# Kernel tuning notes

Hardware: AMD Instinct MI355X
Metric: run time of the kernel (lower is better)

## Reference

```python
import jax, jax.numpy as jnp
import numpy as np

DIM = 512; HEADS = 8; DHEAD = 64; INNER = HEADS * DHEAD
T = 9; H = 16; W = 16; KS = 5; KT = 7
SEQ = T * H * W + 1          # 2305 tokens incl. BOS
GH = 48; GW = 48             # axial grid: sqrt(T*H*W) = 48
B = 2


def _nearby_mask_np():
    """Faithful numpy port of generate_nearby_mask(causal=True). True = masked."""
    te = (KT - 1) // 2
    frame = H * W
    S = T * frame
    pad = KS // 2
    tmpl = (np.arange(KS * KS) >= (KS * KS) // 2).reshape(KS, KS)
    mb = np.ones((S, T, H + 2 * pad, W + 2 * pad), dtype=bool)
    for t in range(T):
        for h in range(H):
            for w in range(W):
                i = t * frame + h * W + w
                mb[i, t, h:h + KS, w:w + KS] = tmpl
                mb[i, max(0, t - te):t, h:h + KS, w:w + KS] = False
    mb = mb[:, :, pad:-pad, pad:-pad].reshape(S, S)
    mb = np.roll(mb, -1, axis=0)
    out = np.ones((S + 1, S + 1), dtype=bool)  # pad 1 row/col of True at top-left
    out[1:, 1:] = mb
    out[0, 0] = False
    return out


def setup_inputs() -> dict:
    key = jax.random.key(0)
    ks = jax.random.split(key, 16)
    inp = {
        "x": jax.random.normal(ks[0], (B, SEQ, DIM), jnp.float32),
        "nearby_mask": jnp.asarray(_nearby_mask_np()),
    }
    i = 1
    for l in range(3):
        for nm in ("Wq", "Wk", "Wv", "Wo"):
            inp[f"{nm}{l}"] = jax.random.normal(ks[i], (DIM, INNER), jnp.float32) * 0.02
            i += 1
        inp[f"bo{l}"] = jnp.zeros((DIM,), jnp.float32)
    return inp


def _neg(dt):
    return -jnp.finfo(dt).max


def _axial(x, Wq, Wk, Wv, Wo, bo, typ):
    # type 0: attend along rows (width axis); type 1: attend along columns.
    b = x.shape[0]
    scale = DHEAD ** -0.5
    q, k, v = x @ Wq, x @ Wk, x @ Wv

    def split(t):
        bos = t[:, :1].reshape(b, 1, HEADS, DHEAD).transpose(0, 2, 1, 3)[:, :, None]  # b hd 1 1 d
        img = t[:, 1:].reshape(b, GH, GW, HEADS, DHEAD)
        if typ == 0:
            img = img.transpose(0, 3, 1, 2, 4)  # b hd h w d
            nq = GH
        else:
            img = img.transpose(0, 3, 2, 1, 4)  # b hd w h d
            nq = GW
        bos = jnp.broadcast_to(bos, (b, HEADS, nq, 1, DHEAD))
        return jnp.concatenate([bos, img], axis=3)  # b hd nq (1+len) d

    qs, ks, vs = split(q), split(k), split(v)
    dots = jnp.einsum('bhnid,bhnjd->bhnij', qs, ks) * scale
    L = dots.shape[-1]
    causal = jnp.triu(jnp.ones((L, L), dtype=bool), 1)
    dots = jnp.where(causal, _neg(dots.dtype), dots)
    attn = jax.nn.softmax(dots, axis=-1)
    out = jnp.einsum('bhnij,bhnjd->bhnid', attn, vs)
    out_bos = out[:, :, 0, 0].reshape(b, 1, INNER)
    oi = out[:, :, :, 1:, :]
    if typ == 0:
        oi = oi.transpose(0, 2, 3, 1, 4).reshape(b, GH * GW, INNER)  # b (h w) (hd d)
    else:
        oi = oi.transpose(0, 3, 2, 1, 4).reshape(b, GH * GW, INNER)
    return jnp.concatenate([out_bos, oi], axis=1) @ Wo + bo


def _nearby(x, Wq, Wk, Wv, Wo, bo, mask):
    b, n, _ = x.shape
    scale = DHEAD ** -0.5
    q = (x @ Wq).reshape(b, n, HEADS, DHEAD).transpose(0, 2, 1, 3)
    k = (x @ Wk).reshape(b, n, HEADS, DHEAD).transpose(0, 2, 1, 3)
    v = (x @ Wv).reshape(b, n, HEADS, DHEAD).transpose(0, 2, 1, 3)
    dots = jnp.einsum('bhid,bhjd->bhij', q, k) * scale
    dots = jnp.where(mask, _neg(dots.dtype), dots)
    attn = jax.nn.softmax(dots, axis=-1)
    out = jnp.einsum('bhij,bhjd->bhid', attn, v)
    return out.transpose(0, 2, 1, 3).reshape(b, n, INNER) @ Wo + bo


def reference(x, nearby_mask,
              Wq0, Wk0, Wv0, Wo0, bo0,
              Wq1, Wk1, Wv1, Wo1, bo1,
              Wq2, Wk2, Wv2, Wo2, bo2):
    x = x + _axial(x, Wq0, Wk0, Wv0, Wo0, bo0, 0)   # row axial
    x = x + _axial(x, Wq1, Wk1, Wv1, Wo1, bo1, 1)   # column axial
    x = x + _nearby(x, Wq2, Wk2, Wv2, Wo2, bo2, nearby_mask)  # nearby sparse-mask attn
    return x
```

## Files before the change

kernel.cpp:

```cpp
#include <hip/hip_runtime.h>
#include <hip/hip_bf16.h>

#define SEQ 2305
#define NROWS 4610
#define MPAD 4736
#define DIM 512
#define QKVN 1536

typedef __attribute__((ext_vector_type(8))) short v8s;
typedef __attribute__((ext_vector_type(4))) float v4f;

__device__ __forceinline__ float bf2f(unsigned short u) {
    return __uint_as_float(((unsigned)u) << 16);
}

__device__ __forceinline__ void load_lds16(const void* g, void* l) {
    __builtin_amdgcn_global_load_lds(
        (const __attribute__((address_space(1))) void*)g,
        (__attribute__((address_space(3))) void*)l, 16, 0, 0);
}

struct WPack { const float* p[12]; };

__global__ void prep_inputs(WPack wp, __hip_bfloat16* __restrict__ wqkv,
                            __hip_bfloat16* __restrict__ wo,
                            const float4* __restrict__ xin,
                            __hip_bfloat16* __restrict__ xb, int n4,
                            float* __restrict__ colsum) {
    int tx = threadIdx.x, ty = threadIdx.y;
    int m = blockIdx.z;
    if (m == 12) {
        int tidl = ty * 32 + tx;
        int bid = blockIdx.y * 16 + blockIdx.x;
        if (bid == 0) {
            #pragma unroll
            for (int k = 0; k < 4; k++) colsum[k * 256 + tidl] = 0.f;
        }
        for (int i = bid * 256 + tidl; i < n4; i += 65536) {
            float4 v = xin[i];
            int j = i * 4;
            xb[j + 0] = __float2bfloat16(v.x);
            xb[j + 1] = __float2bfloat16(v.y);
            xb[j + 2] = __float2bfloat16(v.z);
            xb[j + 3] = __float2bfloat16(v.w);
        }
        return;
    }
    __shared__ float tile[32][33];
    const float* src = wp.p[m];
    int l = m >> 2, j = m & 3;
    __hip_bfloat16* dst = (j < 3) ? (wqkv + (size_t)l * QKVN * DIM + (size_t)j * DIM * DIM)
                                  : (wo + (size_t)l * DIM * DIM);
    int bx = blockIdx.x * 32, by = blockIdx.y * 32;
    #pragma unroll
    for (int i = 0; i < 4; i++)
        tile[ty + 8 * i][tx] = src[(size_t)(by + ty + 8 * i) * DIM + bx + tx];
    __syncthreads();
    #pragma unroll
    for (int i = 0; i < 4; i++)
        dst[(size_t)(bx + ty + 8 * i) * DIM + by + tx] = __float2bfloat16(tile[tx][ty + 8 * i]);
}

__global__ __launch_bounds__(256) void gemm_lds(
    const __hip_bfloat16* __restrict__ A, const __hip_bfloat16* __restrict__ Bt,
    float* __restrict__ C, const float* __restrict__ bias,
    const __hip_bfloat16* __restrict__ resb, __hip_bfloat16* __restrict__ Cb,
    int M, int N, float* __restrict__ colsum) {
    __shared__ short As[2][64 * 32];
    __shared__ short Bs[2][128 * 32];
    const int K = 512;
    int tid = threadIdx.x;
    int wid = tid >> 6, lane = tid & 63;
    int quad = lane >> 4, l16 = lane & 15;
    int bM = blockIdx.x * 64, bN = blockIdx.y * 128;
    int wM = (wid >> 1) * 32, wN = (wid & 1) * 64;

    const short* Ag = (const short*)A;
    const short* Bg = (const short*)Bt;

    int rowS = tid >> 2, cg = tid & 3;
    const short* gA = Ag + (size_t)(bM + rowS) * K + cg * 8;
    const short* gB0 = Bg + (size_t)(bN + rowS) * K + cg * 8;
    const short* gB1 = Bg + (size_t)(bN + 64 + rowS) * K + cg * 8;

    v4f acc[2][4] = {};
    for (int k0 = 0; k0 < K; k0 += 64) {
        #pragma unroll
        for (int s = 0; s < 2; s++) {
            load_lds16(gA + k0 + s * 32, As[s] + wid * 512);
            load_lds16(gB0 + k0 + s * 32, Bs[s] + wid * 512);
            load_lds16(gB1 + k0 + s * 32, Bs[s] + 2048 + wid * 512);
        }
        __syncthreads();
        #pragma unroll
        for (int s = 0; s < 2; s++) {
            v8s af[2], bf[4];
            #pragma unroll
            for (int i = 0; i < 2; i++)
                af[i] = *(const v8s*)(As[s] + (wM + i * 16 + l16) * 32 + quad * 8);
            #pragma unroll
            for (int j = 0; j < 4; j++)
                bf[j] = *(const v8s*)(Bs[s] + (wN + j * 16 + l16) * 32 + quad * 8);
            #pragma unroll
            for (int i = 0; i < 2; i++)
                #pragma unroll
                for (int j = 0; j < 4; j++)
                    acc[i][j] = __builtin_amdgcn_mfma_f32_16x16x32_bf16(af[i], bf[j], acc[i][j], 0, 0, 0);
        }
        __syncthreads();
    }

    const unsigned short* resu = (const unsigned short*)resb;
    #pragma unroll
    for (int i = 0; i < 2; i++) {
        int row = bM + wM + i * 16 + quad * 4;
        #pragma unroll
        for (int j = 0; j < 4; j++) {
            int col = bN + wN + j * 16 + l16;
            #pragma unroll
            for (int r = 0; r < 4; r++) {
                int rr = row + r;
                if (rr < M) {
                    float v = acc[i][j][r];
                    if (bias) v += bias[col];
                    size_t idx = (size_t)rr * N + col;
                    if (resu) v += bf2f(resu[idx]);
                    if (C) C[idx] = v;
                    if (Cb) Cb[idx] = __float2bfloat16(v);
                }
            }
        }
    }

    if (colsum) {
        #pragma unroll
        for (int j = 0; j < 4; j++) {
            int col = bN + wN + j * 16 + l16;
            if (col >= 1024) {
                float s0 = 0.f, s1 = 0.f;
                #pragma unroll
                for (int i = 0; i < 2; i++) {
                    int row = bM + wM + i * 16 + quad * 4;
                    #pragma unroll
                    for (int r = 0; r < 4; r++) {
                        int rr = row + r;
                        if (rr < M) {
                            float v = acc[i][j][r];
                            if (rr >= SEQ) s1 += v; else s0 += v;
                        }
                    }
                }
                s0 += __shfl_xor(s0, 16); s0 += __shfl_xor(s0, 32);
                s1 += __shfl_xor(s1, 16); s1 += __shfl_xor(s1, 32);
                if (quad == 0) {
                    if (s0 != 0.f) atomicAdd(&colsum[col - 1024], s0);
                    if (s1 != 0.f) atomicAdd(&colsum[512 + col - 1024], s1);
                }
            }
        }
    }
}

__global__ __launch_bounds__(256) void axial_flash(
    const unsigned short* __restrict__ qkvb, __hip_bfloat16* __restrict__ attn_b, int typ) {
    __shared__ short Ks[64 * 64];
    __shared__ short Vs[64 * 64];
    __shared__ short Ps[64 * 72];
    __shared__ float invl[64];

    int tid = threadIdx.x;
    int wid = tid >> 6, lane = tid & 63;
    int quad = lane >> 4, l16 = lane & 15;
    int n = blockIdx.x;
    int b = blockIdx.y >> 3, h = blockIdx.y & 7;
    size_t rowbase = (size_t)b * SEQ;
    int hoff = h * 64;

    #pragma unroll
    for (int it = 0; it < 2; it++) {
        int linear = it * 256 + tid;
        int slot = linear >> 3;
        int cd = linear & 7;
        int cs = cd ^ (slot & 7);
        int sp = (slot == 0) ? 0
               : (slot <= 48 ? (typ == 0 ? 1 + n * 48 + (slot - 1) : 1 + (slot - 1) * 48 + n) : 0);
        const unsigned short* srcK = qkvb + (rowbase + sp) * QKVN + hoff + 512 + cs * 8;
        load_lds16(srcK, Ks + it * 2048 + wid * 512 + lane * 8);
        const unsigned short* srcV = qkvb + (rowbase + sp) * QKVN + hoff + 1024 + cd * 8;
        load_lds16(srcV, Vs + it * 2048 + wid * 512 + lane * 8);
    }

    int qi = wid * 16 + l16;
    int sp_q = (qi >= 1 && qi <= 48)
             ? (typ == 0 ? 1 + n * 48 + (qi - 1) : 1 + (qi - 1) * 48 + n) : 0;
    const unsigned short* qptr = qkvb + (rowbase + sp_q) * QKVN + hoff + quad * 8;
    v8s qa0 = *(const v8s*)qptr;
    v8s qa1 = *(const v8s*)(qptr + 32);

    __syncthreads();

    if (n == 0 && tid < 64) {
        attn_b[rowbase * DIM + hoff + tid] =
            __float2bfloat16(bf2f(qkvb[rowbase * QKVN + hoff + 1024 + tid]));
    }

    v4f st[4];
    #pragma unroll
    for (int kt = 0; kt < 4; kt++) {
        int slot = kt * 16 + l16;
        int s7 = slot & 7;
        v8s blo = *(const v8s*)(Ks + slot * 64 + ((quad ^ s7) * 8));
        v8s bhi = *(const v8s*)(Ks + slot * 64 + (((4 + quad) ^ s7) * 8));
        v4f a = {};
        a = __builtin_amdgcn_mfma_f32_16x16x32_bf16(qa0, blo, a, 0, 0, 0);
        a = __builtin_amdgcn_mfma_f32_16x16x32_bf16(qa1, bhi, a, 0, 0, 0);
        st[kt] = a;
    }

    const float NEG = -3.0e38f;
    float sv[4][4];
    float pm[4] = {NEG, NEG, NEG, NEG};
    #pragma unroll
    for (int kt = 0; kt < 4; kt++) {
        int j = kt * 16 + l16;
        #pragma unroll
        for (int r = 0; r < 4; r++) {
            int i = wid * 16 + quad * 4 + r;
            bool ok = (i >= 1) && (i <= 48) && (j <= i);
            float v = ok ? st[kt][r] * 0.125f : NEG;
            sv[kt][r] = v;
            pm[r] = fmaxf(pm[r], v);
        }
    }
    #pragma unroll
    for (int r = 0; r < 4; r++)
        for (int o = 1; o < 16; o <<= 1) pm[r] = fmaxf(pm[r], __shfl_xor(pm[r], o));

    float ps[4] = {0.f, 0.f, 0.f, 0.f};
    #pragma unroll
    for (int kt = 0; kt < 4; kt++) {
        int j = kt * 16 + l16;
        #pragma unroll
        for (int r = 0; r < 4; r++) {
            float e = __expf(sv[kt][r] - pm[r]);
            ps[r] += e;
            Ps[(wid * 16 + quad * 4 + r) * 72 + j] = (short)__bfloat16_as_ushort(__float2bfloat16(e));
        }
    }
    #pragma unroll
    for (int r = 0; r < 4; r++)
        for (int o = 1; o < 16; o <<= 1) ps[r] += __shfl_xor(ps[r], o);
    if (l16 == 0) {
        #pragma unroll
        for (int r = 0; r < 4; r++)
            invl[wid * 16 + quad * 4 + r] = 1.0f / ps[r];
    }
    __syncthreads();

    #pragma unroll
    for (int qt = 0; qt < 4; qt++) {
        v4f oc = {};
        #pragma unroll
        for (int kc = 0; kc < 2; kc++) {
            v8s pa = *(const v8s*)(Ps + (qt * 16 + l16) * 72 + kc * 32 + quad * 8);
            v8s bfr;
            #pragma unroll
            for (int jj = 0; jj < 8; jj++)
                bfr[jj] = Vs[(kc * 32 + quad * 8 + jj) * 64 + wid * 16 + l16];
            oc = __builtin_amdgcn_mfma_f32_16x16x32_bf16(pa, bfr, oc, 0, 0, 0);
        }
        #pragma unroll
        for (int r = 0; r < 4; r++) {
            int i = qt * 16 + quad * 4 + r;
            if (i >= 1 && i <= 48) {
                int sp = typ == 0 ? 1 + n * 48 + (i - 1) : 1 + (i - 1) * 48 + n;
                attn_b[(rowbase + sp) * DIM + hoff + wid * 16 + l16] =
                    __float2bfloat16(oc[r] * invl[i]);
            }
        }
    }
}

__global__ __launch_bounds__(256) void nearby_flash(
    const unsigned short* __restrict__ qkvb, const float* __restrict__ colsum,
    __hip_bfloat16* __restrict__ attn_b) {
    __shared__ short Vs[128 * 64];
    __shared__ __hip_bfloat16 Ps[16 * 264];
    __shared__ float redm[16 * 4];
    __shared__ float reds[16 * 4];

    int tid = threadIdx.x;
    int wid = tid >> 6, lane = tid & 63;
    int quad = lane >> 4, l16 = lane & 15;

    int idx = blockIdx.x;
    if (idx >= 2304) {
        int b = idx - 2304;
        size_t rb = (size_t)b * SEQ;
        for (int c = tid; c < 512; c += 256) {
            attn_b[(rb + 2304) * DIM + c] =
                __float2bfloat16(colsum[b * 512 + c] * (1.0f / 2305.0f));
            attn_b[rb * DIM + c] =
                __float2bfloat16(bf2f(qkvb[rb * QKVN + 1024 + c]));
        }
        return;
    }

    int bh = idx & 15;
    int tile = idx >> 4;
    int b = bh >> 3, h = bh & 7;
    int t = tile >> 4;
    int sxy = tile & 15;
    int hh0 = (sxy >> 2) * 4, ww0 = (sxy & 3) * 4;
    int nf = (t < 3 ? t : 3) + 1;
    int t0 = t - (nf - 1);
    size_t rowbase = (size_t)b * SEQ;
    int hoff = h * 64;

    auto slot_kp = [&](int slot) -> int {
        int f = slot >> 6, uy = (slot >> 3) & 7, ux = slot & 7;
        int kh = hh0 - 2 + uy, kw = ww0 - 2 + ux;
        int kt = t0 + f;
        bool ok = (kh >= 0) && (kh < 16) && (kw >= 0) && (kw < 16) && (f < nf);
        return ok ? (kt * 256 + kh * 16 + kw + 1) : 0;
    };

    int qp_f = t * 256 + (hh0 + (l16 >> 2)) * 16 + (ww0 + (l16 & 3));
    const unsigned short* qptr = qkvb + (rowbase + qp_f) * QKVN + hoff + quad * 8;
    v8s qa0 = *(const v8s*)qptr;
    v8s qa1 = *(const v8s*)(qptr + 32);

    v8s kb_lo[4], kb_hi[4];
    #pragma unroll
    for (int k = 0; k < 4; k++) {
        int slot = (wid * 4 + k) * 16 + l16;
        int kp = slot_kp(slot);
        const unsigned short* kr = qkvb + (rowbase + kp) * QKVN + hoff + 512;
        kb_lo[k] = *(const v8s*)(kr + quad * 8);
        kb_hi[k] = *(const v8s*)(kr + 32 + quad * 8);
    }

    #pragma unroll
    for (int it = 0; it < 4; it++) {
        int linear = it * 256 + tid;
        int slot = linear >> 3;
        int cd = linear & 7;
        int cs = cd ^ ((slot >> 3) & 7);
        int kp = slot_kp(slot);
        const unsigned short* src = qkvb + (rowbase + kp) * QKVN + hoff + 1024 + cs * 8;
        load_lds16(src, Vs + it * 2048 + wid * 512 + lane * 8);
    }

    v4f st[4];
    #pragma unroll
    for (int k = 0; k < 4; k++) {
        v4f a = {};
        a = __builtin_amdgcn_mfma_f32_16x16x32_bf16(qa0, kb_lo[k], a, 0, 0, 0);
        a = __builtin_amdgcn_mfma_f32_16x16x32_bf16(qa1, kb_hi[k], a, 0, 0, 0);
        st[k] = a;
    }

    const float NEG = -3.0e38f;
    float sv[4][4];
    float pm[4] = {NEG, NEG, NEG, NEG};
    #pragma unroll
    for (int k = 0; k < 4; k++) {
        int slot = (wid * 4 + k) * 16 + l16;
        int f = slot >> 6, uy = (slot >> 3) & 7, ux = slot & 7;
        int kh = hh0 - 2 + uy, kw = ww0 - 2 + ux;
        bool okb = (kh >= 0) && (kh < 16) && (kw >= 0) && (kw < 16) && (f < nf);
        int dyp2 = uy - quad;
        bool oky = okb && (dyp2 >= 0) && (dyp2 <= 4);
        #pragma unroll
        for (int r = 0; r < 4; r++) {
            int dxp2 = ux - r;
            bool ok = oky && (dxp2 >= 0) && (dxp2 <= 4);
            if (f == nf - 1) ok = ok && (dyp2 * 5 + dxp2 < 12);
            float v = ok ? st[k][r] * 0.125f : NEG;
            sv[k][r] = v;
            pm[r] = fmaxf(pm[r], v);
        }
    }
    #pragma unroll
    for (int r = 0; r < 4; r++)
        for (int o = 1; o < 16; o <<= 1) pm[r] = fmaxf(pm[r], __shfl_xor(pm[r], o));
    if (l16 == 0) {
        #pragma unroll
        for (int r = 0; r < 4; r++) redm[(quad * 4 + r) * 4 + wid] = pm[r];
    }
    __syncthreads();

    float rm[4];
    #pragma unroll
    for (int r = 0; r < 4; r++) {
        int row = (quad * 4 + r) * 4;
        rm[r] = fmaxf(fmaxf(redm[row], redm[row + 1]), fmaxf(redm[row + 2], redm[row + 3]));
    }

    float ps[4] = {0.f, 0.f, 0.f, 0.f};
    #pragma unroll
    for (int k = 0; k < 4; k++) {
        int slot = (wid * 4 + k) * 16 + l16;
        #pragma unroll
        for (int r = 0; r < 4; r++) {
            float e = __expf(sv[k][r] - rm[r]);
            ps[r] += e;
            Ps[(quad * 4 + r) * 264 + slot] = __float2bfloat16(e);
        }
    }
    #pragma unroll
    for (int r = 0; r < 4; r++)
        for (int o = 1; o < 16; o <<= 1) ps[r] += __shfl_xor(ps[r], o);
    if (l16 == 0) {
        #pragma unroll
        for (int r = 0; r < 4; r++) reds[(quad * 4 + r) * 4 + wid] = ps[r];
    }
    __syncthreads();

    float inv[4];
    #pragma unroll
    for (int r = 0; r < 4; r++) {
        int row = (quad * 4 + r) * 4;
        float d = reds[row] + reds[row + 1] + reds[row + 2] + reds[row + 3];
        inv[r] = 1.0f / d;
    }

    int dcol = wid * 16 + l16;
    int c_r = dcol >> 3, d7 = dcol & 7;
    v4f oc = {};
    #pragma unroll
    for (int kc = 0; kc < 4; kc++) {
        v8s pa = *(const v8s*)((const short*)Ps + l16 * 264 + kc * 32 + quad * 8);
        v8s bf;
        #pragma unroll
        for (int j = 0; j < 8; j++) {
            int slot = kc * 32 + quad * 8 + j;
            int key = (slot >> 3) & 7;
            bf[j] = Vs[(slot & 127) * 64 + ((c_r ^ key) * 8) + d7];
        }
        oc = __builtin_amdgcn_mfma_f32_16x16x32_bf16(pa, bf, oc, 0, 0, 0);
    }
    __syncthreads();

    #pragma unroll
    for (int it = 0; it < 4; it++) {
        int linear = 1024 + it * 256 + tid;
        int slot = linear >> 3;
        int cd = linear & 7;
        int cs = cd ^ ((slot >> 3) & 7);
        int kp = slot_kp(slot);
        const unsigned short* src = qkvb + (rowbase + kp) * QKVN + hoff + 1024 + cs * 8;
        load_lds16(src, Vs + it * 2048 + wid * 512 + lane * 8);
    }
    __syncthreads();

    #pragma unroll
    for (int kc = 4; kc < 8; kc++) {
        v8s pa = *(const v8s*)((const short*)Ps + l16 * 264 + kc * 32 + quad * 8);
        v8s bf;
        #pragma unroll
        for (int j = 0; j < 8; j++) {
            int slot = kc * 32 + quad * 8 + j;
            int key = (slot >> 3) & 7;
            bf[j] = Vs[(slot & 127) * 64 + ((c_r ^ key) * 8) + d7];
        }
        oc = __builtin_amdgcn_mfma_f32_16x16x32_bf16(pa, bf, oc, 0, 0, 0);
    }

    #pragma unroll
    for (int r = 0; r < 4; r++) {
        int qp = t * 256 + (hh0 + quad) * 16 + (ww0 + r);
        if (qp != 0) {
            attn_b[(rowbase + qp) * DIM + hoff + dcol] =
                __float2bfloat16(oc[r] * inv[r]);
        }
    }
}

extern "C" void kernel_launch(void* const* d_in, const int* in_sizes, int n_in,
                              void* d_out, int out_size, void* d_ws, size_t ws_size,
                              hipStream_t stream) {
    const float* x = (const float*)d_in[0];
    float* xcur = (float*)d_out;

    char* ws = (char*)d_ws;
    size_t off = 0;
    auto alloc = [&](size_t bytes) -> void* {
        void* p = ws + off;
        off = (off + bytes + 255) & ~(size_t)255;
        return p;
    };
    __hip_bfloat16* wqkv  = (__hip_bfloat16*)alloc((size_t)3 * QKVN * DIM * 2);
    __hip_bfloat16* wo    = (__hip_bfloat16*)alloc((size_t)3 * DIM * DIM * 2);
    __hip_bfloat16* xb    = (__hip_bfloat16*)alloc((size_t)MPAD * DIM * 2);
    __hip_bfloat16* attnb = (__hip_bfloat16*)alloc((size_t)MPAD * DIM * 2);
    float* colsum         = (float*)alloc((size_t)2 * 512 * 4);
    __hip_bfloat16* qkvb  = (__hip_bfloat16*)alloc((size_t)NROWS * QKVN * 2);

    const int nElem = NROWS * DIM;
    const int n4 = nElem / 4;

    WPack wp;
    for (int l = 0; l < 3; l++)
        for (int j = 0; j < 4; j++)
            wp.p[l * 4 + j] = (const float*)d_in[2 + l * 5 + j];
    prep_inputs<<<dim3(16, 16, 13), dim3(32, 8), 0, stream>>>(
        wp, wqkv, wo, (const float4*)x, xb, n4, colsum);

    for (int l = 0; l < 3; l++) {
        gemm_lds<<<dim3(MPAD / 64, QKVN / 128), 256, 0, stream>>>(
            xb, wqkv + (size_t)l * QKVN * DIM, nullptr, nullptr, nullptr, qkvb,
            NROWS, QKVN, l == 2 ? colsum : nullptr);
        if (l < 2) {
            axial_flash<<<dim3(48, 16), 256, 0, stream>>>((const unsigned short*)qkvb, attnb, l);
        } else {
            nearby_flash<<<2304 + 2, 256, 0, stream>>>(
                (const unsigned short*)qkvb, colsum, attnb);
        }
        const float* bo = (const float*)d_in[6 + l * 5];
        if (l < 2) {
            gemm_lds<<<dim3(MPAD / 64, DIM / 128), 256, 0, stream>>>(
                attnb, wo + (size_t)l * DIM * DIM, nullptr, bo, xb, xb, NROWS, DIM, nullptr);
        } else {
            gemm_lds<<<dim3(MPAD / 64, DIM / 128), 256, 0, stream>>>(
                attnb, wo + (size_t)l * DIM * DIM, xcur, bo, xb, nullptr, NROWS, DIM, nullptr);
        }
    }
}
```

Baseline: 260.3 us.

## Fuse all layer stages into one persistent cooperative kernel with grid syncs

Replaces the nine separate launches (QKV GEMM, attention, output GEMM per layer) with a single persistent cooperative kernel. The blocks loop over tiles of each stage and use grid.sync between stages, and the stage bodies become noinline device functions that share one LDS buffer. This targets per-launch overhead and inter-kernel gaps. In exchange the grid is capped by occupancy, so per-stage parallelism is limited, the noinline calls may raise register pressure, and the grid barriers add their own cost. A fallback path with separate launches is kept in case the cooperative launch fails.

```diff
diff --git a/kernel.cpp b/kernel.cpp
--- a/kernel.cpp
+++ b/kernel.cpp
@@ -1,11 +1,15 @@
 #include <hip/hip_runtime.h>
 #include <hip/hip_bf16.h>
+#include <hip/hip_cooperative_groups.h>
+
+namespace cg = cooperative_groups;
 
 #define SEQ 2305
 #define NROWS 4610
 #define MPAD 4736
 #define DIM 512
 #define QKVN 1536
+#define SMEM_BYTES 25856
 
 typedef __attribute__((ext_vector_type(8))) short v8s;
 typedef __attribute__((ext_vector_type(4))) float v4f;
@@ -21,6 +25,7 @@
 }
 
 struct WPack { const float* p[12]; };
+struct BPack { const float* bo[3]; };
 
 __global__ void prep_inputs(WPack wp, __hip_bfloat16* __restrict__ wqkv,
                             __hip_bfloat16* __restrict__ wo,
@@ -61,46 +66,52 @@
         dst[(size_t)(bx + ty + 8 * i) * DIM + by + tx] = __float2bfloat16(tile[tx][ty + 8 * i]);
 }
 
-__global__ __launch_bounds__(256) void gemm_lds(
-    const __hip_bfloat16* __restrict__ A, const __hip_bfloat16* __restrict__ Bt,
-    float* __restrict__ C, const float* __restrict__ bias,
-    const __hip_bfloat16* __restrict__ resb, __hip_bfloat16* __restrict__ Cb,
-    int M, int N, float* __restrict__ colsum) {
-    __shared__ short As[2][64 * 32];
-    __shared__ short Bs[2][128 * 32];
+
+__device__ __attribute__((noinline)) void gemm_body(
+    char* smemc,
+    const __hip_bfloat16* A, const __hip_bfloat16* Bt,
+    float* C, const float* bias,
+    const __hip_bfloat16* resb, __hip_bfloat16* Cb,
+    int M, int N, float* colsum, int v, int tilesX) {
+    short* As0 = (short*)smemc;
+    short* As1 = As0 + 2048;
+    short* Bs0 = As1 + 2048;
+    short* Bs1 = Bs0 + 4096;
     const int K = 512;
     int tid = threadIdx.x;
     int wid = tid >> 6, lane = tid & 63;
     int quad = lane >> 4, l16 = lane & 15;
-    int bM = blockIdx.x * 64, bN = blockIdx.y * 128;
+    int bM = (v % tilesX) * 64, bN = (v / tilesX) * 128;
     int wM = (wid >> 1) * 32, wN = (wid & 1) * 64;
 
     const short* Ag = (const short*)A;
     const short* Bg = (const short*)Bt;
 
-    int rowS = tid >> 2, cg = tid & 3;
-    const short* gA = Ag + (size_t)(bM + rowS) * K + cg * 8;
-    const short* gB0 = Bg + (size_t)(bN + rowS) * K + cg * 8;
-    const short* gB1 = Bg + (size_t)(bN + 64 + rowS) * K + cg * 8;
+    int rowS = tid >> 2, cg0 = tid & 3;
+    const short* gA = Ag + (size_t)(bM + rowS) * K + cg0 * 8;
+    const short* gB0 = Bg + (size_t)(bN + rowS) * K + cg0 * 8;
+    const short* gB1 = Bg + (size_t)(bN + 64 + rowS) * K + cg0 * 8;
 
     v4f acc[2][4] = {};
     for (int k0 = 0; k0 < K; k0 += 64) {
+        load_lds16(gA + k0, As0 + wid * 512);
+        load_lds16(gB0 + k0, Bs0 + wid * 512);
+        load_lds16(gB1 + k0, Bs0 + 2048 + wid * 512);
+        load_lds16(gA + k0 + 32, As1 + wid * 512);
+        load_lds16(gB0 + k0 + 32, Bs1 + wid * 512);
+        load_lds16(gB1 + k0 + 32, Bs1 + 2048 + wid * 512);
+        __syncthreads();
         #pragma unroll
         for (int s = 0; s < 2; s++) {
-            load_lds16(gA + k0 + s * 32, As[s] + wid * 512);
-            load_lds16(gB0 + k0 + s * 32, Bs[s] + wid * 512);
-            load_lds16(gB1 + k0 + s * 32, Bs[s] + 2048 + wid * 512);
-        }
-        __syncthreads();
-        #pragma unroll
-        for (int s = 0; s < 2; s++) {
+            const short* Asp = s ? As1 : As0;
+            const short* Bsp = s ? Bs1 : Bs0;
             v8s af[2], bf[4];
             #pragma unroll
             for (int i = 0; i < 2; i++)
-                af[i] = *(const v8s*)(As[s] + (wM + i * 16 + l16) * 32 + quad * 8);
+                af[i] = *(const v8s*)(Asp + (wM + i * 16 + l16) * 32 + quad * 8);
             #pragma unroll
             for (int j = 0; j < 4; j++)
-                bf[j] = *(const v8s*)(Bs[s] + (wN + j * 16 + l16) * 32 + quad * 8);
+                bf[j] = *(const v8s*)(Bsp + (wN + j * 16 + l16) * 32 + quad * 8);
             #pragma unroll
             for (int i = 0; i < 2; i++)
                 #pragma unroll
@@ -121,12 +132,12 @@
             for (int r = 0; r < 4; r++) {
                 int rr = row + r;
                 if (rr < M) {
-                    float v = acc[i][j][r];
-                    if (bias) v += bias[col];
+                    float vv = acc[i][j][r];
+                    if (bias) vv += bias[col];
                     size_t idx = (size_t)rr * N + col;
-                    if (resu) v += bf2f(resu[idx]);
-                    if (C) C[idx] = v;
-                    if (Cb) Cb[idx] = __float2bfloat16(v);
+                    if (resu) vv += bf2f(resu[idx]);
+                    if (C) C[idx] = vv;
+                    if (Cb) Cb[idx] = __float2bfloat16(vv);
                 }
             }
         }
@@ -145,8 +156,8 @@
                     for (int r = 0; r < 4; r++) {
                         int rr = row + r;
                         if (rr < M) {
-                            float v = acc[i][j][r];
-                            if (rr >= SEQ) s1 += v; else s0 += v;
+                            float vv = acc[i][j][r];
+                            if (rr >= SEQ) s1 += vv; else s0 += vv;
                         }
                     }
                 }
@@ -161,20 +172,23 @@
     }
 }
 
-__global__ __launch_bounds__(256) void axial_flash(
-    const unsigned short* __restrict__ qkvb, __hip_bfloat16* __restrict__ attn_b, int typ) {
-    __shared__ short Ks[64 * 64];
-    __shared__ short Vs[64 * 64];
-    __shared__ short Ps[64 * 72];
-    __shared__ float invl[64];
+__device__ __attribute__((noinline)) void axial_body(
+    char* smemc, const unsigned short* qkvb, __hip_bfloat16* attn_b, int typ, int v) {
+    short* Ks = (short*)smemc;
+    short* Vs = Ks + 4096;
+    short* Ps = Vs + 4096;
+    float* invl = (float*)(smemc + 25600);
 
     int tid = threadIdx.x;
     int wid = tid >> 6, lane = tid & 63;
     int quad = lane >> 4, l16 = lane & 15;
-    int n = blockIdx.x;
-    int b = blockIdx.y >> 3, h = blockIdx.y & 7;
+    int n = v % 48;
+    int bh = v / 48;
+    int b = bh >> 3, h = bh & 7;
     size_t rowbase = (size_t)b * SEQ;
     int hoff = h * 64;
+
+    __syncthreads();
 
     #pragma unroll
     for (int it = 0; it < 2; it++) {
@@ -227,9 +241,9 @@
         for (int r = 0; r < 4; r++) {
             int i = wid * 16 + quad * 4 + r;
             bool ok = (i >= 1) && (i <= 48) && (j <= i);
-            float v = ok ? st[kt][r] * 0.125f : NEG;
-            sv[kt][r] = v;
-            pm[r] = fmaxf(pm[r], v);
+            float vv = ok ? st[kt][r] * 0.125f : NEG;
+            sv[kt][r] = vv;
+            pm[r] = fmaxf(pm[r], vv);
         }
     }
     #pragma unroll
@@ -281,21 +295,20 @@
     }
 }
 
-__global__ __launch_bounds__(256) void nearby_flash(
-    const unsigned short* __restrict__ qkvb, const float* __restrict__ colsum,
-    __hip_bfloat16* __restrict__ attn_b) {
-    __shared__ short Vs[128 * 64];
-    __shared__ __hip_bfloat16 Ps[16 * 264];
-    __shared__ float redm[16 * 4];
-    __shared__ float reds[16 * 4];
+__device__ __attribute__((noinline)) void nearby_body(
+    char* smemc, const unsigned short* qkvb, const float* colsum,
+    __hip_bfloat16* attn_b, int v) {
+    short* Vs = (short*)smemc;
+    __hip_bfloat16* Ps = (__hip_bfloat16*)(smemc + 16384);
+    float* redm = (float*)(smemc + 24832);
+    float* reds = redm + 64;
 
     int tid = threadIdx.x;
     int wid = tid >> 6, lane = tid & 63;
     int quad = lane >> 4, l16 = lane & 15;
 
-    int idx = blockIdx.x;
-    if (idx >= 2304) {
-        int b = idx - 2304;
+    if (v >= 2304) {
+        int b = v - 2304;
         size_t rb = (size_t)b * SEQ;
         for (int c = tid; c < 512; c += 256) {
             attn_b[(rb + 2304) * DIM + c] =
@@ -306,8 +319,8 @@
         return;
     }
 
-    int bh = idx & 15;
-    int tile = idx >> 4;
+    int bh = v & 15;
+    int tile = v >> 4;
     int b = bh >> 3, h = bh & 7;
     int t = tile >> 4;
     int sxy = tile & 15;
@@ -325,6 +338,8 @@
         return ok ? (kt * 256 + kh * 16 + kw + 1) : 0;
     };
 
+    __syncthreads();
+
     int qp_f = t * 256 + (hh0 + (l16 >> 2)) * 16 + (ww0 + (l16 & 3));
     const unsigned short* qptr = qkvb + (rowbase + qp_f) * QKVN + hoff + quad * 8;
     v8s qa0 = *(const v8s*)qptr;
@@ -376,9 +391,9 @@
             int dxp2 = ux - r;
             bool ok = oky && (dxp2 >= 0) && (dxp2 <= 4);
             if (f == nf - 1) ok = ok && (dyp2 * 5 + dxp2 < 12);
-            float v = ok ? st[k][r] * 0.125f : NEG;
-            sv[k][r] = v;
-            pm[r] = fmaxf(pm[r], v);
+            float vv = ok ? st[k][r] * 0.125f : NEG;
+            sv[k][r] = vv;
+            pm[r] = fmaxf(pm[r], vv);
         }
     }
     #pragma unroll
@@ -475,6 +490,58 @@
                 __float2bfloat16(oc[r] * inv[r]);
         }
     }
+}
+
+__global__ __launch_bounds__(256) void fused_layers(
+    __hip_bfloat16* xb, const __hip_bfloat16* wqkv, const __hip_bfloat16* wo,
+    __hip_bfloat16* qkvb, __hip_bfloat16* attnb, float* colsum, float* xcur, BPack bp) {
+    __shared__ __align__(16) char smem[SMEM_BYTES];
+    cg::grid_group grid = cg::this_grid();
+    const int G = gridDim.x;
+    for (int l = 0; l < 3; l++) {
+        const __hip_bfloat16* wq = wqkv + (size_t)l * QKVN * DIM;
+        for (int v = blockIdx.x; v < 74 * 12; v += G)
+            gemm_body(smem, xb, wq, nullptr, nullptr, nullptr, qkvb, NROWS, QKVN,
+                      (l == 2) ? colsum : nullptr, v, 74);
+        __threadfence();
+        grid.sync();
+        if (l < 2) {
+            for (int v = blockIdx.x; v < 768; v += G)
+                axial_body(smem, (const unsigned short*)qkvb, attnb, l, v);
+        } else {
+            for (int v = blockIdx.x; v < 2306; v += G)
+                nearby_body(smem, (const unsigned short*)qkvb, colsum, attnb, v);
+        }
+        __threadfence();
+        grid.sync();
+        const __hip_bfloat16* wl = wo + (size_t)l * DIM * DIM;
+        if (l < 2) {
+            for (int v = blockIdx.x; v < 74 * 4; v += G)
+                gemm_body(smem, attnb, wl, nullptr, bp.bo[l], xb, xb, NROWS, DIM, nullptr, v, 74);
+            __threadfence();
+            grid.sync();
+        } else {
+            for (int v = blockIdx.x; v < 74 * 4; v += G)
+                gemm_body(smem, attnb, wl, xcur, bp.bo[2], xb, nullptr, NROWS, DIM, nullptr, v, 74);
+        }
+    }
+}
+
+__global__ __launch_bounds__(256) void gemm_k(
+    const __hip_bfloat16* A, const __hip_bfloat16* Bt, float* C, const float* bias,
+    const __hip_bfloat16* resb, __hip_bfloat16* Cb, int M, int N, float* colsum, int tilesX) {
+    __shared__ __align__(16) char smem[24576];
+    gemm_body(smem, A, Bt, C, bias, resb, Cb, M, N, colsum, blockIdx.x, tilesX);
+}
+__global__ __launch_bounds__(256) void axial_k(
+    const unsigned short* qkvb, __hip_bfloat16* attn_b, int typ) {
+    __shared__ __align__(16) char smem[SMEM_BYTES];
+    axial_body(smem, qkvb, attn_b, typ, blockIdx.x);
+}
+__global__ __launch_bounds__(256) void nearby_k(
+    const unsigned short* qkvb, const float* colsum, __hip_bfloat16* attn_b) {
+    __shared__ __align__(16) char smem[25344];
+    nearby_body(smem, qkvb, colsum, attn_b, blockIdx.x);
 }
 
 extern "C" void kernel_launch(void* const* d_in, const int* in_sizes, int n_in,
@@ -507,23 +574,44 @@
     prep_inputs<<<dim3(16, 16, 13), dim3(32, 8), 0, stream>>>(
         wp, wqkv, wo, (const float4*)x, xb, n4, colsum);
 
-    for (int l = 0; l < 3; l++) {
-        gemm_lds<<<dim3(MPAD / 64, QKVN / 128), 256, 0, stream>>>(
-            xb, wqkv + (size_t)l * QKVN * DIM, nullptr, nullptr, nullptr, qkvb,
-            NROWS, QKVN, l == 2 ? colsum : nullptr);
-        if (l < 2) {
-            axial_flash<<<dim3(48, 16), 256, 0, stream>>>((const unsigned short*)qkvb, attnb, l);
-        } else {
-            nearby_flash<<<2304 + 2, 256, 0, stream>>>(
-                (const unsigned short*)qkvb, colsum, attnb);
-        }
-        const float* bo = (const float*)d_in[6 + l * 5];
-        if (l < 2) {
-            gemm_lds<<<dim3(MPAD / 64, DIM / 128), 256, 0, stream>>>(
-                attnb, wo + (size_t)l * DIM * DIM, nullptr, bo, xb, xb, NROWS, DIM, nullptr);
-        } else {
-            gemm_lds<<<dim3(MPAD / 64, DIM / 128), 256, 0, stream>>>(
-                attnb, wo + (size_t)l * DIM * DIM, xcur, bo, xb, nullptr, NROWS, DIM, nullptr);
-        }
-    }
-}
+    BPack bp;
+    for (int l = 0; l < 3; l++) bp.bo[l] = (const float*)d_in[6 + l * 5];
+
+    hipError_t err = hipErrorUnknown;
+    int nb = 0;
+    if (hipOccupancyMaxActiveBlocksPerMultiprocessor(&nb, fused_layers, 256, 0) == hipSuccess
+        && nb > 0) {
+        hipDeviceProp_t prop;
+        int dev = 0;
+        hipGetDevice(&dev);
+        if (hipGetDeviceProperties(&prop, dev) == hipSuccess) {
+            int G = nb * prop.multiProcessorCount;
+            if (G > 2306) G = 2306;
+            void* args[] = { (void*)&xb, (void*)&wqkv, (void*)&wo, (void*)&qkvb,
+                             (void*)&attnb, (void*)&colsum, (void*)&xcur, (void*)&bp };
+            err = hipLaunchCooperativeKernel((void*)fused_layers, dim3(G), dim3(256),
+                                             args, 0, stream);
+        }
+    }
+    if (err != hipSuccess) {
+        for (int l = 0; l < 3; l++) {
+            gemm_k<<<74 * 12, 256, 0, stream>>>(
+                xb, wqkv + (size_t)l * QKVN * DIM, nullptr, nullptr, nullptr, qkvb,
+                NROWS, QKVN, l == 2 ? colsum : nullptr, 74);
+            if (l < 2) {
+                axial_k<<<768, 256, 0, stream>>>((const unsigned short*)qkvb, attnb, l);
+            } else {
+                nearby_k<<<2306, 256, 0, stream>>>((const unsigned short*)qkvb, colsum, attnb);
+            }
+            if (l < 2) {
+                gemm_k<<<74 * 4, 256, 0, stream>>>(
+                    attnb, wo + (size_t)l * DIM * DIM, nullptr, bp.bo[l], xb, xb,
+                    NROWS, DIM, nullptr, 74);
+            } else {
+                gemm_k<<<74 * 4, 256, 0, stream>>>(
+                    attnb, wo + (size_t)l * DIM * DIM, xcur, bp.bo[2], xb, nullptr,
+                    NROWS, DIM, nullptr, 74);
+            }
+        }
+    }
+}
```

Result: slower. 822.2 us (+215.9%).
